# Performance work log

Measured on AMD Instinct MI355X. Metric: run time of the kernel, lower is better.

## Reference

```python
import jax, jax.numpy as jnp
import numpy as np

B, T, C = 128, 256, 256
K1, S1, T1 = 2, 2, 128   # conv scale 1: kernel, stride, output time steps
K2, S2, T2 = 4, 4, 64    # conv scale 2
TT = T + T1 + T2         # 448, concatenated time dim fed to TriU
EPS = 1e-5


def hardswish(x):
    return x * jnp.clip(x + 3.0, 0.0, 6.0) / 6.0


def setup_inputs() -> dict:
    key = jax.random.key(0)
    ks = jax.random.split(key, 9)
    return {
        "x": jax.random.normal(ks[0], (B, T, C), jnp.float32),
        "conv_w1": jax.random.normal(ks[1], (C, C, K1), jnp.float32) * 0.05,
        "conv_b1": jax.random.normal(ks[2], (C,), jnp.float32) * 0.05,
        "conv_w2": jax.random.normal(ks[3], (C, C, K2), jnp.float32) * 0.05,
        "conv_b2": jax.random.normal(ks[4], (C,), jnp.float32) * 0.05,
        "ln1_g": jnp.ones((T1, C), jnp.float32),
        "ln1_b": jnp.zeros((T1, C), jnp.float32),
        "ln2_g": jnp.ones((T2, C), jnp.float32),
        "ln2_b": jnp.zeros((T2, C), jnp.float32),
        "triu_w1": jax.random.normal(ks[5], (TT, TT), jnp.float32) * 0.05,
        "triu_b1": jax.random.normal(ks[6], (TT,), jnp.float32) * 0.05,
        "triu_w2": jax.random.normal(ks[7], (TT, TT), jnp.float32) * 0.05,
        "triu_b2": jax.random.normal(ks[8], (TT,), jnp.float32) * 0.05,
    }


def _layernorm2(x, g, b):
    # nn.LayerNorm([ts, C]): normalize jointly over last two dims of [B, ts, C]
    mu = jnp.mean(x, axis=(-2, -1), keepdims=True)
    var = jnp.var(x, axis=(-2, -1), keepdims=True)
    return (x - mu) * jax.lax.rsqrt(var + EPS) * g + b


def _conv1d(x_bct, w, b, stride):
    # x: [B, C, T], w: [Cout, Cin, K] -> [B, Cout, T_out], VALID padding
    y = jax.lax.conv_general_dilated(
        x_bct, w, window_strides=(stride,), padding='VALID',
        dimension_numbers=('NCH', 'OIH', 'NCH'))
    return y + b[None, :, None]


def reference(x, conv_w1, conv_b1, conv_w2, conv_b2,
              ln1_g, ln1_b, ln2_g, ln2_b,
              triu_w1, triu_b1, triu_w2, triu_b2):
    xc = jnp.transpose(x, (0, 2, 1))  # [B, C, T]
    f1 = _layernorm2(jnp.transpose(_conv1d(xc, conv_w1, conv_b1, S1), (0, 2, 1)), ln1_g, ln1_b)
    f2 = _layernorm2(jnp.transpose(_conv1d(xc, conv_w2, conv_b2, S2), (0, 2, 1)), ln2_g, ln2_b)
    cat = jnp.concatenate([x, f1, f2], axis=1)  # [B, TT, C]
    # TriU network on time axis: per-step Linear(i+1,1) == upper-triangular matmul
    z = jnp.transpose(cat, (0, 2, 1))  # [B, C, TT]
    mask = jnp.triu(jnp.ones((TT, TT), z.dtype))  # M[j,i]=w_i[j] for j<=i
    z = hardswish(z @ (triu_w1 * mask) + triu_b1)
    z = z @ (triu_w2 * mask) + triu_b2
    return jnp.transpose(z, (0, 2, 1))  # [B, TT, C]
```

## Files before the change

### kernel.cpp

```cpp
#include <hip/hip_runtime.h>
#include <hip/hip_bf16.h>

#define Bn   128
#define Tn   256
#define Cn   256
#define T1n  128
#define T2n  64
#define TTn  448
#define EPSf 1e-5f

typedef __attribute__((ext_vector_type(8))) short short8;
typedef __attribute__((ext_vector_type(4))) short short4v;
typedef __attribute__((ext_vector_type(4))) float f32x4;

__device__ __forceinline__ unsigned short f2b(float f) {
    union { __hip_bfloat16 h; unsigned short u; } cv;
    cv.h = __float2bfloat16(f);
    return cv.u;
}

__device__ __forceinline__ short8 cvt8(float4 a, float4 b) {
    short8 r;
    r[0] = (short)f2b(a.x); r[1] = (short)f2b(a.y); r[2] = (short)f2b(a.z); r[3] = (short)f2b(a.w);
    r[4] = (short)f2b(b.x); r[5] = (short)f2b(b.y); r[6] = (short)f2b(b.z); r[7] = (short)f2b(b.w);
    return r;
}

__global__ __launch_bounds__(256) void prep_all(
        const float* __restrict__ cw1, const float* __restrict__ cw2,
        const float* __restrict__ tw1, const float* __restrict__ tw2,
        const float* __restrict__ ln1g, const float* __restrict__ ln1b,
        const float* __restrict__ ln2g, const float* __restrict__ ln2b,
        unsigned short* __restrict__ w1rT, unsigned short* __restrict__ w2rT,
        unsigned short* __restrict__ wm1b, unsigned short* __restrict__ wm2b,
        float* __restrict__ gt1, float* __restrict__ bt1,
        float* __restrict__ gt2, float* __restrict__ bt2) {
    int idx = blockIdx.x * 256 + threadIdx.x;
    if (idx < 131072) {
        int co = idx >> 9, r = idx & 511, k = r >> 8, ci = r & 255;
        w1rT[idx] = f2b(cw1[(size_t)co * 512 + ci * 2 + k]);
    } else if ((idx -= 131072) < 262144) {
        int co = idx >> 10, r = idx & 1023, k = r >> 8, ci = r & 255;
        w2rT[idx] = f2b(cw2[(size_t)co * 1024 + ci * 4 + k]);
    } else if ((idx -= 262144) < 200704) {
        int i = idx / TTn, j = idx % TTn;
        wm1b[idx] = (j <= i) ? f2b(tw1[(size_t)j * TTn + i]) : (unsigned short)0;
    } else if ((idx -= 200704) < 200704) {
        int i = idx / TTn, j = idx % TTn;
        wm2b[idx] = (j <= i) ? f2b(tw2[(size_t)j * TTn + i]) : (unsigned short)0;
    } else if ((idx -= 200704) < 32768) {
        int c = idx >> 7, r = idx & 127;
        gt1[idx] = ln1g[(size_t)r * Cn + c];
    } else if ((idx -= 32768) < 32768) {
        int c = idx >> 7, r = idx & 127;
        bt1[idx] = ln1b[(size_t)r * Cn + c];
    } else if ((idx -= 32768) < 16384) {
        int c = idx >> 6, r = idx & 63;
        gt2[idx] = ln2g[(size_t)r * Cn + c];
    } else if ((idx -= 16384) < 16384) {
        int c = idx >> 6, r = idx & 63;
        bt2[idx] = ln2b[(size_t)r * Cn + c];
    }
}

__global__ __launch_bounds__(256) void xpose_kernel(const float* __restrict__ x,
                                                    unsigned short* __restrict__ catb) {
    __shared__ float tl[64][65];
    int b = blockIdx.z, t0 = blockIdx.y * 64, c0 = blockIdx.x * 64;
    const float* xp = x + (size_t)b * Tn * Cn;
    int lr = threadIdx.x >> 4;
    int lc = (threadIdx.x & 15) * 4;
#pragma unroll
    for (int rr = 0; rr < 4; ++rr) {
        int row = lr + rr * 16;
        float4 v = *(const float4*)(xp + (size_t)(t0 + row) * Cn + c0 + lc);
        tl[lc + 0][row] = v.x; tl[lc + 1][row] = v.y;
        tl[lc + 2][row] = v.z; tl[lc + 3][row] = v.w;
    }
    __syncthreads();
    int cr = threadIdx.x >> 2, tq = (threadIdx.x & 3) * 16;
    unsigned short* qp = catb + (size_t)b * (TTn * Cn) + (size_t)(c0 + cr) * TTn + t0 + tq;
    short8 o0, o1;
#pragma unroll
    for (int j = 0; j < 8; ++j) {
        o0[j] = (short)f2b(tl[cr][tq + j]);
        o1[j] = (short)f2b(tl[cr][tq + 8 + j]);
    }
    *(short8*)(qp) = o0;
    *(short8*)(qp + 8) = o1;
}

__global__ __launch_bounds__(256) void ln_apply_both(
        const float* __restrict__ c1t, const float* __restrict__ c2t,
        const float* __restrict__ gt1, const float* __restrict__ bt1,
        const float* __restrict__ gt2, const float* __restrict__ bt2,
        const float* __restrict__ ps1, const float* __restrict__ ps2,
        unsigned short* __restrict__ catb) {
    const int b = blockIdx.y, bx = blockIdx.x;
    const float *p, *g, *be;
    unsigned short* q;
    int LG, n, base;
    float S = 0.f, SS = 0.f;
    if (bx < 16) {
        n = Cn * T1n; LG = 7;
        p = c1t + (size_t)b * n; g = gt1; be = bt1;
        q = catb + (size_t)b * (TTn * Cn) + Tn;
#pragma unroll
        for (int s_ = 0; s_ < 4; ++s_) { S += ps1[b * 8 + s_ * 2]; SS += ps1[b * 8 + s_ * 2 + 1]; }
        base = bx * 2048;
    } else {
        n = Cn * T2n; LG = 6;
        p = c2t + (size_t)b * n; g = gt2; be = bt2;
        q = catb + (size_t)b * (TTn * Cn) + Tn + T1n;
#pragma unroll
        for (int s_ = 0; s_ < 2; ++s_) { S += ps2[b * 4 + s_ * 2]; SS += ps2[b * 4 + s_ * 2 + 1]; }
        base = (bx - 16) * 2048;
    }
    float mu = S / n;
    float rs = rsqrtf(SS / n - mu * mu + EPSf);

    int i = base + threadIdx.x * 8;
    int c = i >> LG, t = i & ((1 << LG) - 1);
    float4 v0 = *(const float4*)(p + i);
    float4 v1 = *(const float4*)(p + i + 4);
    float4 g0 = *(const float4*)(g + i);
    float4 g1 = *(const float4*)(g + i + 4);
    float4 b0 = *(const float4*)(be + i);
    float4 b1 = *(const float4*)(be + i + 4);
    float4 o0, o1;
    o0.x = fmaf((v0.x - mu) * rs, g0.x, b0.x);
    o0.y = fmaf((v0.y - mu) * rs, g0.y, b0.y);
    o0.z = fmaf((v0.z - mu) * rs, g0.z, b0.z);
    o0.w = fmaf((v0.w - mu) * rs, g0.w, b0.w);
    o1.x = fmaf((v1.x - mu) * rs, g1.x, b1.x);
    o1.y = fmaf((v1.y - mu) * rs, g1.y, b1.y);
    o1.z = fmaf((v1.z - mu) * rs, g1.z, b1.z);
    o1.w = fmaf((v1.w - mu) * rs, g1.w, b1.w);
    *(short8*)(q + (size_t)c * TTn + t) = cvt8(o0, o1);
}

template<bool AF32, int EPI>
__global__ __launch_bounds__(256)
void gemm_mfma(const void* __restrict__ Av, long astride, int lda,
               const unsigned short* __restrict__ Bsrc, long bstride, int ldb,
               const float* __restrict__ bias,
               void* __restrict__ Cv, long cstride, int ldc,
               int K, float* __restrict__ psout) {
    const int tid = threadIdx.x;
    const int lane = tid & 63;
    const int wid = tid >> 6;
    const int wr = wid >> 1, wc = wid & 1;
    const int bz = blockIdx.z;
    const int m0 = blockIdx.y * 64, n0 = blockIdx.x * 128;

    __shared__ unsigned short As[64 * 64];
    __shared__ unsigned short Bs[128 * 64];
    char* AsB = (char*)As;
    char* BsB = (char*)Bs;

    const int ar = tid >> 2, akq = tid & 3;
    const int bn_ = tid >> 1, bkh = (tid & 1) * 32;

    const float* Afp = (const float*)Av + (size_t)bz * astride + (size_t)(m0 + ar) * lda + akq * 16;
    const unsigned short* Ahp = (const unsigned short*)Av + (size_t)bz * astride + (size_t)(m0 + ar) * lda + akq * 16;
    const unsigned short* Bp = Bsrc + (size_t)bz * bstride + (size_t)(n0 + bn_) * ldb + bkh;

    const int awb = ar * 128 + akq * 32;
    const int aswz = (ar & 7) << 4;
    const int bwb = bn_ * 128 + bkh * 2;
    const int bswz = (bn_ & 7) << 4;

    short8 ra0, ra1, rb0, rb1, rb2, rb3;

    auto loadA = [&](int k0) {
        if constexpr (AF32) {
            const float* p = Afp + k0;
            float4 v0 = *(const float4*)(p);
            float4 v1 = *(const float4*)(p + 4);
            float4 v2 = *(const float4*)(p + 8);
            float4 v3 = *(const float4*)(p + 12);
            ra0 = cvt8(v0, v1);
            ra1 = cvt8(v2, v3);
        } else {
            ra0 = *(const short8*)(Ahp + k0);
            ra1 = *(const short8*)(Ahp + k0 + 8);
        }
    };
    auto loadB = [&](int k0) {
        rb0 = *(const short8*)(Bp + k0);
        rb1 = *(const short8*)(Bp + k0 + 8);
        rb2 = *(const short8*)(Bp + k0 + 16);
        rb3 = *(const short8*)(Bp + k0 + 24);
    };
    auto stage = [&]() {
        *(short8*)(AsB + ((awb) ^ aswz)) = ra0;
        *(short8*)(AsB + ((awb + 16) ^ aswz)) = ra1;
        *(short8*)(BsB + ((bwb) ^ bswz)) = rb0;
        *(short8*)(BsB + ((bwb + 16) ^ bswz)) = rb1;
        *(short8*)(BsB + ((bwb + 32) ^ bswz)) = rb2;
        *(short8*)(BsB + ((bwb + 48) ^ bswz)) = rb3;
    };

    const int fl = lane & 15;
    const int fkb = (lane >> 4) * 16;
    const int amb = (wr * 32 + fl) * 128;
    const int bnb = (wc * 64 + fl) * 128;
    const int fswz = (fl & 7) << 4;

    f32x4 acc[2][4];
#pragma unroll
    for (int i = 0; i < 2; ++i)
#pragma unroll
        for (int j = 0; j < 4; ++j) acc[i][j] = (f32x4){0.f, 0.f, 0.f, 0.f};

    const int nkt = (EPI == 0) ? (K >> 6) : ((m0 >> 6) + 1);

    loadA(0);
    loadB(0);
    for (int kt = 0; kt < nkt; ++kt) {
        __syncthreads();
        stage();
        __syncthreads();
        if (kt + 1 < nkt) { loadA((kt + 1) * 64); loadB((kt + 1) * 64); }
#pragma unroll
        for (int ks = 0; ks < 2; ++ks) {
            const int kb = ks * 64 + fkb;
            short8 af0 = *(const short8*)(AsB + ((amb + kb) ^ fswz));
            short8 af1 = *(const short8*)(AsB + ((amb + 2048 + kb) ^ fswz));
            short8 bf0 = *(const short8*)(BsB + ((bnb + kb) ^ fswz));
            short8 bf1 = *(const short8*)(BsB + ((bnb + 2048 + kb) ^ fswz));
            short8 bf2 = *(const short8*)(BsB + ((bnb + 4096 + kb) ^ fswz));
            short8 bf3 = *(const short8*)(BsB + ((bnb + 6144 + kb) ^ fswz));
            acc[0][0] = __builtin_amdgcn_mfma_f32_16x16x32_bf16(af0, bf0, acc[0][0], 0, 0, 0);
            acc[0][1] = __builtin_amdgcn_mfma_f32_16x16x32_bf16(af0, bf1, acc[0][1], 0, 0, 0);
            acc[0][2] = __builtin_amdgcn_mfma_f32_16x16x32_bf16(af0, bf2, acc[0][2], 0, 0, 0);
            acc[0][3] = __builtin_amdgcn_mfma_f32_16x16x32_bf16(af0, bf3, acc[0][3], 0, 0, 0);
            acc[1][0] = __builtin_amdgcn_mfma_f32_16x16x32_bf16(af1, bf0, acc[1][0], 0, 0, 0);
            acc[1][1] = __builtin_amdgcn_mfma_f32_16x16x32_bf16(af1, bf1, acc[1][1], 0, 0, 0);
            acc[1][2] = __builtin_amdgcn_mfma_f32_16x16x32_bf16(af1, bf2, acc[1][2], 0, 0, 0);
            acc[1][3] = __builtin_amdgcn_mfma_f32_16x16x32_bf16(af1, bf3, acc[1][3], 0, 0, 0);
        }
    }

    const int lrow = (lane >> 4) * 4;
    float s_ = 0.f, ss_ = 0.f;
#pragma unroll
    for (int mf = 0; mf < 2; ++mf) {
        const int trow = m0 + wr * 32 + mf * 16 + lrow;
#pragma unroll
        for (int nf = 0; nf < 4; ++nf) {
            const int col = n0 + wc * 64 + nf * 16 + fl;
            f32x4 v = acc[mf][nf];
            if (EPI == 0) {
                v += bias[col];
#pragma unroll
                for (int r = 0; r < 4; ++r) { s_ += v[r]; ss_ = fmaf(v[r], v[r], ss_); }
                float* Cb = (float*)Cv + (size_t)bz * cstride + (size_t)col * ldc + trow;
                *(f32x4*)Cb = v;
            } else if (EPI == 1) {
                f32x4 bv = *(const f32x4*)(bias + trow);
                v += bv;
                unsigned short* Cb = (unsigned short*)Cv + (size_t)bz * cstride + (size_t)col * ldc + trow;
                short4v pk;
#pragma unroll
                for (int r = 0; r < 4; ++r) {
                    float t = v[r];
                    float u = fminf(fmaxf(t + 3.f, 0.f), 6.f);
                    t = t * u * (1.f / 6.f);
                    pk[r] = (short)f2b(t);
                }
                *(short4v*)Cb = pk;
            } else {
                f32x4 bv = *(const f32x4*)(bias + trow);
                v += bv;
                float* Cb = (float*)Cv + (size_t)bz * cstride + (size_t)trow * ldc + col;
#pragma unroll
                for (int r = 0; r < 4; ++r) Cb[(size_t)r * ldc] = v[r];
            }
        }
    }

    if (EPI == 0) {
#pragma unroll
        for (int o = 32; o > 0; o >>= 1) { s_ += __shfl_down(s_, o); ss_ += __shfl_down(ss_, o); }
        __shared__ float rsm[8];
        if (lane == 0) { rsm[wid] = s_; rsm[wid + 4] = ss_; }
        __syncthreads();
        if (tid == 0) {
            float S = rsm[0] + rsm[1] + rsm[2] + rsm[3];
            float SS = rsm[4] + rsm[5] + rsm[6] + rsm[7];
            int nslots = gridDim.x * gridDim.y;
            int slot = blockIdx.y * gridDim.x + blockIdx.x;
            psout[((size_t)bz * nslots + slot) * 2 + 0] = S;
            psout[((size_t)bz * nslots + slot) * 2 + 1] = SS;
        }
    }
}

extern "C" void kernel_launch(void* const* d_in, const int* in_sizes, int n_in,
                              void* d_out, int out_size, void* d_ws, size_t ws_size,
                              hipStream_t stream) {
    const float* x    = (const float*)d_in[0];
    const float* cw1  = (const float*)d_in[1];
    const float* cb1  = (const float*)d_in[2];
    const float* cw2  = (const float*)d_in[3];
    const float* cb2  = (const float*)d_in[4];
    const float* ln1g = (const float*)d_in[5];
    const float* ln1b = (const float*)d_in[6];
    const float* ln2g = (const float*)d_in[7];
    const float* ln2b = (const float*)d_in[8];
    const float* tw1  = (const float*)d_in[9];
    const float* tb1  = (const float*)d_in[10];
    const float* tw2  = (const float*)d_in[11];
    const float* tb2  = (const float*)d_in[12];
    float* out = (float*)d_out;

    char* w = (char*)d_ws;
    unsigned short* catb = (unsigned short*)w;
    unsigned short* z1b  = (unsigned short*)(w + 29360128);
    float*          c1t  = (float*)(w + 58720256);
    float*          c2t  = (float*)(w + 75497472);
    unsigned short* w1rT = (unsigned short*)(w + 83886080);
    unsigned short* w2rT = (unsigned short*)(w + 84148224);
    unsigned short* wm1b = (unsigned short*)(w + 84672512);
    unsigned short* wm2b = (unsigned short*)(w + 85073920);
    float*          gt1  = (float*)(w + 85475328);
    float*          bt1  = (float*)(w + 85606400);
    float*          gt2  = (float*)(w + 85737472);
    float*          bt2  = (float*)(w + 85803008);
    float*          ps1  = (float*)(w + 85868544);
    float*          ps2  = (float*)(w + 85876736);

    prep_all<<<3488, 256, 0, stream>>>(cw1, cw2, tw1, tw2, ln1g, ln1b, ln2g, ln2b,
                                       w1rT, w2rT, wm1b, wm2b, gt1, bt1, gt2, bt2);

    xpose_kernel<<<dim3(4, 4, Bn), 256, 0, stream>>>(x, catb);

    gemm_mfma<true, 0><<<dim3(2, 2, Bn), 256, 0, stream>>>(
        x, 65536L, 512, w1rT, 0L, 512, cb1, c1t, (long)Cn * T1n, T1n, 512, ps1);
    gemm_mfma<true, 0><<<dim3(2, 1, Bn), 256, 0, stream>>>(
        x, 65536L, 1024, w2rT, 0L, 1024, cb2, c2t, (long)Cn * T2n, T2n, 1024, ps2);

    ln_apply_both<<<dim3(24, Bn), 256, 0, stream>>>(c1t, c2t, gt1, bt1, gt2, bt2, ps1, ps2, catb);

    gemm_mfma<false, 1><<<dim3(2, 7, Bn), 256, 0, stream>>>(
        wm1b, 0L, TTn, catb, (long)TTn * Cn, TTn, tb1, z1b, (long)TTn * Cn, TTn, TTn, nullptr);

    gemm_mfma<false, 2><<<dim3(2, 7, Bn), 256, 0, stream>>>(
        wm2b, 0L, TTn, z1b, (long)TTn * Cn, TTn, tb2, out, (long)TTn * Cn, Cn, TTn, nullptr);
}
```

Before: 113.6 us.

## Fuse transpose and conv GEMMs into one launch; use 128x128 tiles for TriU GEMMs

Merges the x transpose kernel and both strided-conv GEMMs into a single stage1 launch that dispatches on blockIdx.y, which removes two kernel launches and lets the three pieces of work run concurrently. The TriU GEMMs move from 64x128 to 128x128 tiles with a 4x4 MFMA fragment per wave, raising data reuse per block. To support this, the masked weight matrices are padded to 512 rows with zeros and the workspace offsets are shifted. The larger tile uses more registers and LDS and skips less of the triangular work, since it works at 128-row granularity.

New measurement: 141.6 us. 24.7% more time.

```diff
diff --git a/kernel.cpp b/kernel.cpp
--- a/kernel.cpp
+++ b/kernel.cpp
@@ -42,13 +42,13 @@
     } else if ((idx -= 131072) < 262144) {
         int co = idx >> 10, r = idx & 1023, k = r >> 8, ci = r & 255;
         w2rT[idx] = f2b(cw2[(size_t)co * 1024 + ci * 4 + k]);
-    } else if ((idx -= 262144) < 200704) {
+    } else if ((idx -= 262144) < 229376) {
         int i = idx / TTn, j = idx % TTn;
-        wm1b[idx] = (j <= i) ? f2b(tw1[(size_t)j * TTn + i]) : (unsigned short)0;
-    } else if ((idx -= 200704) < 200704) {
+        wm1b[idx] = (i < TTn && j <= i) ? f2b(tw1[(size_t)j * TTn + i]) : (unsigned short)0;
+    } else if ((idx -= 229376) < 229376) {
         int i = idx / TTn, j = idx % TTn;
-        wm2b[idx] = (j <= i) ? f2b(tw2[(size_t)j * TTn + i]) : (unsigned short)0;
-    } else if ((idx -= 200704) < 32768) {
+        wm2b[idx] = (i < TTn && j <= i) ? f2b(tw2[(size_t)j * TTn + i]) : (unsigned short)0;
+    } else if ((idx -= 229376) < 32768) {
         int c = idx >> 7, r = idx & 127;
         gt1[idx] = ln1g[(size_t)r * Cn + c];
     } else if ((idx -= 32768) < 32768) {
@@ -63,10 +63,11 @@
     }
 }
 
-__global__ __launch_bounds__(256) void xpose_kernel(const float* __restrict__ x,
-                                                    unsigned short* __restrict__ catb) {
-    __shared__ float tl[64][65];
-    int b = blockIdx.z, t0 = blockIdx.y * 64, c0 = blockIdx.x * 64;
+
+__device__ __forceinline__ void xpose_body(char* smem, const float* __restrict__ x,
+                                           unsigned short* __restrict__ catb,
+                                           int b, int t0, int c0) {
+    float (*tl)[65] = (float(*)[65])smem;
     const float* xp = x + (size_t)b * Tn * Cn;
     int lr = threadIdx.x >> 4;
     int lc = (threadIdx.x & 15) * 4;
@@ -88,6 +89,145 @@
     }
     *(short8*)(qp) = o0;
     *(short8*)(qp + 8) = o1;
+}
+
+__device__ __forceinline__ void conv_body(char* smem,
+        const float* __restrict__ x, int lda,
+        const unsigned short* __restrict__ Bw,
+        const float* __restrict__ bias,
+        float* __restrict__ Cout, long cstride, int ldc, int K,
+        float* __restrict__ psout, int slot, int nslots,
+        int m0, int n0, int bz) {
+    char* AsB = smem;
+    char* BsB = smem + 8192;
+    const int tid = threadIdx.x;
+    const int lane = tid & 63;
+    const int wid = tid >> 6;
+    const int wr = wid >> 1, wc = wid & 1;
+
+    const int ar = tid >> 2, akq = tid & 3;
+    const int bn_ = tid >> 1, bkh = (tid & 1) * 32;
+
+    const float* Afp = x + (size_t)bz * (Tn * Cn) + (size_t)(m0 + ar) * lda + akq * 16;
+    const unsigned short* Bp = Bw + (size_t)(n0 + bn_) * K + bkh;
+
+    const int awb = ar * 128 + akq * 32;
+    const int aswz = (ar & 7) << 4;
+    const int bwb = bn_ * 128 + bkh * 2;
+    const int bswz = (bn_ & 7) << 4;
+
+    short8 ra0, ra1, rb0, rb1, rb2, rb3;
+    auto loadA = [&](int k0) {
+        const float* p = Afp + k0;
+        float4 v0 = *(const float4*)(p);
+        float4 v1 = *(const float4*)(p + 4);
+        float4 v2 = *(const float4*)(p + 8);
+        float4 v3 = *(const float4*)(p + 12);
+        ra0 = cvt8(v0, v1);
+        ra1 = cvt8(v2, v3);
+    };
+    auto loadB = [&](int k0) {
+        rb0 = *(const short8*)(Bp + k0);
+        rb1 = *(const short8*)(Bp + k0 + 8);
+        rb2 = *(const short8*)(Bp + k0 + 16);
+        rb3 = *(const short8*)(Bp + k0 + 24);
+    };
+
+    const int fl = lane & 15;
+    const int fkb = (lane >> 4) * 16;
+    const int amb = (wr * 32 + fl) * 128;
+    const int bnb = (wc * 64 + fl) * 128;
+    const int fswz = (fl & 7) << 4;
+
+    f32x4 acc[2][4];
+#pragma unroll
+    for (int i = 0; i < 2; ++i)
+#pragma unroll
+        for (int j = 0; j < 4; ++j) acc[i][j] = (f32x4){0.f, 0.f, 0.f, 0.f};
+
+    const int nkt = K >> 6;
+    loadA(0); loadB(0);
+    for (int kt = 0; kt < nkt; ++kt) {
+        __syncthreads();
+        *(short8*)(AsB + ((awb) ^ aswz)) = ra0;
+        *(short8*)(AsB + ((awb + 16) ^ aswz)) = ra1;
+        *(short8*)(BsB + ((bwb) ^ bswz)) = rb0;
+        *(short8*)(BsB + ((bwb + 16) ^ bswz)) = rb1;
+        *(short8*)(BsB + ((bwb + 32) ^ bswz)) = rb2;
+        *(short8*)(BsB + ((bwb + 48) ^ bswz)) = rb3;
+        __syncthreads();
+        if (kt + 1 < nkt) { loadA((kt + 1) * 64); loadB((kt + 1) * 64); }
+#pragma unroll
+        for (int ks = 0; ks < 2; ++ks) {
+            const int kb = ks * 64 + fkb;
+            short8 af0 = *(const short8*)(AsB + ((amb + kb) ^ fswz));
+            short8 af1 = *(const short8*)(AsB + ((amb + 2048 + kb) ^ fswz));
+            short8 bf0 = *(const short8*)(BsB + ((bnb + kb) ^ fswz));
+            short8 bf1 = *(const short8*)(BsB + ((bnb + 2048 + kb) ^ fswz));
+            short8 bf2 = *(const short8*)(BsB + ((bnb + 4096 + kb) ^ fswz));
+            short8 bf3 = *(const short8*)(BsB + ((bnb + 6144 + kb) ^ fswz));
+            acc[0][0] = __builtin_amdgcn_mfma_f32_16x16x32_bf16(af0, bf0, acc[0][0], 0, 0, 0);
+            acc[0][1] = __builtin_amdgcn_mfma_f32_16x16x32_bf16(af0, bf1, acc[0][1], 0, 0, 0);
+            acc[0][2] = __builtin_amdgcn_mfma_f32_16x16x32_bf16(af0, bf2, acc[0][2], 0, 0, 0);
+            acc[0][3] = __builtin_amdgcn_mfma_f32_16x16x32_bf16(af0, bf3, acc[0][3], 0, 0, 0);
+            acc[1][0] = __builtin_amdgcn_mfma_f32_16x16x32_bf16(af1, bf0, acc[1][0], 0, 0, 0);
+            acc[1][1] = __builtin_amdgcn_mfma_f32_16x16x32_bf16(af1, bf1, acc[1][1], 0, 0, 0);
+            acc[1][2] = __builtin_amdgcn_mfma_f32_16x16x32_bf16(af1, bf2, acc[1][2], 0, 0, 0);
+            acc[1][3] = __builtin_amdgcn_mfma_f32_16x16x32_bf16(af1, bf3, acc[1][3], 0, 0, 0);
+        }
+    }
+
+    const int lrow = (lane >> 4) * 4;
+    float s_ = 0.f, ss_ = 0.f;
+#pragma unroll
+    for (int mf = 0; mf < 2; ++mf) {
+        const int trow = m0 + wr * 32 + mf * 16 + lrow;
+#pragma unroll
+        for (int nf = 0; nf < 4; ++nf) {
+            const int col = n0 + wc * 64 + nf * 16 + fl;
+            f32x4 v = acc[mf][nf];
+            v += bias[col];
+#pragma unroll
+            for (int r = 0; r < 4; ++r) { s_ += v[r]; ss_ = fmaf(v[r], v[r], ss_); }
+            float* Cb = Cout + (size_t)bz * cstride + (size_t)col * ldc + trow;
+            *(f32x4*)Cb = v;
+        }
+    }
+
+#pragma unroll
+    for (int o = 32; o > 0; o >>= 1) { s_ += __shfl_down(s_, o); ss_ += __shfl_down(ss_, o); }
+    __syncthreads();
+    float* rsm = (float*)smem;
+    if (lane == 0) { rsm[wid] = s_; rsm[wid + 4] = ss_; }
+    __syncthreads();
+    if (tid == 0) {
+        float S = rsm[0] + rsm[1] + rsm[2] + rsm[3];
+        float SS = rsm[4] + rsm[5] + rsm[6] + rsm[7];
+        psout[((size_t)bz * nslots + slot) * 2 + 0] = S;
+        psout[((size_t)bz * nslots + slot) * 2 + 1] = SS;
+    }
+}
+
+__global__ __launch_bounds__(256) void stage1(
+        const float* __restrict__ x,
+        const unsigned short* __restrict__ w1rT, const unsigned short* __restrict__ w2rT,
+        const float* __restrict__ cb1, const float* __restrict__ cb2,
+        float* __restrict__ c1t, float* __restrict__ c2t,
+        unsigned short* __restrict__ catb,
+        float* __restrict__ ps1, float* __restrict__ ps2) {
+    __shared__ alignas(16) char smem[25600];
+    const int y = blockIdx.y, xb = blockIdx.x, bz = blockIdx.z;
+    if (y >= 3) {
+        xpose_body(smem, x, catb, bz, (y - 3) * 64, xb * 64);
+    } else if (y < 2) {
+        if (xb < 2)
+            conv_body(smem, x, 512, w1rT, cb1, c1t, (long)Cn * T1n, T1n, 512,
+                      ps1, y * 2 + xb, 4, y * 64, xb * 128, bz);
+    } else {
+        if (xb < 2)
+            conv_body(smem, x, 1024, w2rT, cb2, c2t, (long)Cn * T2n, T2n, 1024,
+                      ps2, xb, 2, 0, xb * 128, bz);
+    }
 }
 
 __global__ __launch_bounds__(256) void ln_apply_both(
@@ -139,128 +279,91 @@
     *(short8*)(q + (size_t)c * TTn + t) = cvt8(o0, o1);
 }
 
-template<bool AF32, int EPI>
+template<int EPI>
 __global__ __launch_bounds__(256)
-void gemm_mfma(const void* __restrict__ Av, long astride, int lda,
-               const unsigned short* __restrict__ Bsrc, long bstride, int ldb,
-               const float* __restrict__ bias,
-               void* __restrict__ Cv, long cstride, int ldc,
-               int K, float* __restrict__ psout) {
+void gemm128(const unsigned short* __restrict__ Asrc,
+             const unsigned short* __restrict__ Bsrc, long bstride,
+             const float* __restrict__ bias,
+             void* __restrict__ Cv, long cstride) {
     const int tid = threadIdx.x;
     const int lane = tid & 63;
     const int wid = tid >> 6;
     const int wr = wid >> 1, wc = wid & 1;
     const int bz = blockIdx.z;
-    const int m0 = blockIdx.y * 64, n0 = blockIdx.x * 128;
-
-    __shared__ unsigned short As[64 * 64];
+    const int m0 = blockIdx.y * 128, n0 = blockIdx.x * 128;
+
+    __shared__ unsigned short As[128 * 64];
     __shared__ unsigned short Bs[128 * 64];
     char* AsB = (char*)As;
     char* BsB = (char*)Bs;
 
-    const int ar = tid >> 2, akq = tid & 3;
-    const int bn_ = tid >> 1, bkh = (tid & 1) * 32;
-
-    const float* Afp = (const float*)Av + (size_t)bz * astride + (size_t)(m0 + ar) * lda + akq * 16;
-    const unsigned short* Ahp = (const unsigned short*)Av + (size_t)bz * astride + (size_t)(m0 + ar) * lda + akq * 16;
-    const unsigned short* Bp = Bsrc + (size_t)bz * bstride + (size_t)(n0 + bn_) * ldb + bkh;
-
-    const int awb = ar * 128 + akq * 32;
-    const int aswz = (ar & 7) << 4;
-    const int bwb = bn_ * 128 + bkh * 2;
-    const int bswz = (bn_ & 7) << 4;
-
-    short8 ra0, ra1, rb0, rb1, rb2, rb3;
-
-    auto loadA = [&](int k0) {
-        if constexpr (AF32) {
-            const float* p = Afp + k0;
-            float4 v0 = *(const float4*)(p);
-            float4 v1 = *(const float4*)(p + 4);
-            float4 v2 = *(const float4*)(p + 8);
-            float4 v3 = *(const float4*)(p + 12);
-            ra0 = cvt8(v0, v1);
-            ra1 = cvt8(v2, v3);
-        } else {
-            ra0 = *(const short8*)(Ahp + k0);
-            ra1 = *(const short8*)(Ahp + k0 + 8);
-        }
-    };
-    auto loadB = [&](int k0) {
-        rb0 = *(const short8*)(Bp + k0);
-        rb1 = *(const short8*)(Bp + k0 + 8);
-        rb2 = *(const short8*)(Bp + k0 + 16);
-        rb3 = *(const short8*)(Bp + k0 + 24);
-    };
-    auto stage = [&]() {
-        *(short8*)(AsB + ((awb) ^ aswz)) = ra0;
-        *(short8*)(AsB + ((awb + 16) ^ aswz)) = ra1;
-        *(short8*)(BsB + ((bwb) ^ bswz)) = rb0;
-        *(short8*)(BsB + ((bwb + 16) ^ bswz)) = rb1;
-        *(short8*)(BsB + ((bwb + 32) ^ bswz)) = rb2;
-        *(short8*)(BsB + ((bwb + 48) ^ bswz)) = rb3;
+    const int srow = tid >> 1, skh = (tid & 1) * 32;
+    const unsigned short* Ap = Asrc + (size_t)(m0 + srow) * TTn + skh;
+    const unsigned short* Bp = Bsrc + (size_t)bz * bstride + (size_t)(n0 + srow) * TTn + skh;
+    const int swb = srow * 128 + skh * 2;
+    const int sswz = (srow & 7) << 4;
+
+    short8 ra[4], rb[4];
+    auto loadAB = [&](int k0) {
+#pragma unroll
+        for (int j = 0; j < 4; ++j) {
+            ra[j] = *(const short8*)(Ap + k0 + j * 8);
+            rb[j] = *(const short8*)(Bp + k0 + j * 8);
+        }
     };
 
     const int fl = lane & 15;
     const int fkb = (lane >> 4) * 16;
-    const int amb = (wr * 32 + fl) * 128;
-    const int bnb = (wc * 64 + fl) * 128;
     const int fswz = (fl & 7) << 4;
 
-    f32x4 acc[2][4];
-#pragma unroll
-    for (int i = 0; i < 2; ++i)
+    f32x4 acc[4][4];
+#pragma unroll
+    for (int i = 0; i < 4; ++i)
 #pragma unroll
         for (int j = 0; j < 4; ++j) acc[i][j] = (f32x4){0.f, 0.f, 0.f, 0.f};
 
-    const int nkt = (EPI == 0) ? (K >> 6) : ((m0 >> 6) + 1);
-
-    loadA(0);
-    loadB(0);
+    const int nkt = min(7, (m0 >> 6) + 2);
+
+    loadAB(0);
     for (int kt = 0; kt < nkt; ++kt) {
         __syncthreads();
-        stage();
+#pragma unroll
+        for (int j = 0; j < 4; ++j) {
+            *(short8*)(AsB + ((swb + j * 16) ^ sswz)) = ra[j];
+            *(short8*)(BsB + ((swb + j * 16) ^ sswz)) = rb[j];
+        }
         __syncthreads();
-        if (kt + 1 < nkt) { loadA((kt + 1) * 64); loadB((kt + 1) * 64); }
+        if (kt + 1 < nkt) loadAB((kt + 1) * 64);
 #pragma unroll
         for (int ks = 0; ks < 2; ++ks) {
             const int kb = ks * 64 + fkb;
-            short8 af0 = *(const short8*)(AsB + ((amb + kb) ^ fswz));
-            short8 af1 = *(const short8*)(AsB + ((amb + 2048 + kb) ^ fswz));
-            short8 bf0 = *(const short8*)(BsB + ((bnb + kb) ^ fswz));
-            short8 bf1 = *(const short8*)(BsB + ((bnb + 2048 + kb) ^ fswz));
-            short8 bf2 = *(const short8*)(BsB + ((bnb + 4096 + kb) ^ fswz));
-            short8 bf3 = *(const short8*)(BsB + ((bnb + 6144 + kb) ^ fswz));
-            acc[0][0] = __builtin_amdgcn_mfma_f32_16x16x32_bf16(af0, bf0, acc[0][0], 0, 0, 0);
-            acc[0][1] = __builtin_amdgcn_mfma_f32_16x16x32_bf16(af0, bf1, acc[0][1], 0, 0, 0);
-            acc[0][2] = __builtin_amdgcn_mfma_f32_16x16x32_bf16(af0, bf2, acc[0][2], 0, 0, 0);
-            acc[0][3] = __builtin_amdgcn_mfma_f32_16x16x32_bf16(af0, bf3, acc[0][3], 0, 0, 0);
-            acc[1][0] = __builtin_amdgcn_mfma_f32_16x16x32_bf16(af1, bf0, acc[1][0], 0, 0, 0);
-            acc[1][1] = __builtin_amdgcn_mfma_f32_16x16x32_bf16(af1, bf1, acc[1][1], 0, 0, 0);
-            acc[1][2] = __builtin_amdgcn_mfma_f32_16x16x32_bf16(af1, bf2, acc[1][2], 0, 0, 0);
-            acc[1][3] = __builtin_amdgcn_mfma_f32_16x16x32_bf16(af1, bf3, acc[1][3], 0, 0, 0);
+            short8 af[4], bf[4];
+#pragma unroll
+            for (int mf = 0; mf < 4; ++mf)
+                af[mf] = *(const short8*)(AsB + (((wr * 64 + mf * 16 + fl) * 128 + kb) ^ fswz));
+#pragma unroll
+            for (int nf = 0; nf < 4; ++nf)
+                bf[nf] = *(const short8*)(BsB + (((wc * 64 + nf * 16 + fl) * 128 + kb) ^ fswz));
+#pragma unroll
+            for (int mf = 0; mf < 4; ++mf)
+#pragma unroll
+                for (int nf = 0; nf < 4; ++nf)
+                    acc[mf][nf] = __builtin_amdgcn_mfma_f32_16x16x32_bf16(af[mf], bf[nf], acc[mf][nf], 0, 0, 0);
         }
     }
 
     const int lrow = (lane >> 4) * 4;
-    float s_ = 0.f, ss_ = 0.f;
-#pragma unroll
-    for (int mf = 0; mf < 2; ++mf) {
-        const int trow = m0 + wr * 32 + mf * 16 + lrow;
+#pragma unroll
+    for (int mf = 0; mf < 4; ++mf) {
+        const int trow = m0 + wr * 64 + mf * 16 + lrow;
+        if (trow >= TTn) continue;
+        f32x4 bv = *(const f32x4*)(bias + trow);
 #pragma unroll
         for (int nf = 0; nf < 4; ++nf) {
             const int col = n0 + wc * 64 + nf * 16 + fl;
-            f32x4 v = acc[mf][nf];
-            if (EPI == 0) {
-                v += bias[col];
-#pragma unroll
-                for (int r = 0; r < 4; ++r) { s_ += v[r]; ss_ = fmaf(v[r], v[r], ss_); }
-                float* Cb = (float*)Cv + (size_t)bz * cstride + (size_t)col * ldc + trow;
-                *(f32x4*)Cb = v;
-            } else if (EPI == 1) {
-                f32x4 bv = *(const f32x4*)(bias + trow);
-                v += bv;
-                unsigned short* Cb = (unsigned short*)Cv + (size_t)bz * cstride + (size_t)col * ldc + trow;
+            f32x4 v = acc[mf][nf] + bv;
+            if (EPI == 1) {
+                unsigned short* Cb = (unsigned short*)Cv + (size_t)bz * cstride + (size_t)col * TTn + trow;
                 short4v pk;
 #pragma unroll
                 for (int r = 0; r < 4; ++r) {
@@ -271,28 +374,10 @@
                 }
                 *(short4v*)Cb = pk;
             } else {
-                f32x4 bv = *(const f32x4*)(bias + trow);
-                v += bv;
-                float* Cb = (float*)Cv + (size_t)bz * cstride + (size_t)trow * ldc + col;
-#pragma unroll
-                for (int r = 0; r < 4; ++r) Cb[(size_t)r * ldc] = v[r];
+                float* Cb = (float*)Cv + (size_t)bz * cstride + (size_t)trow * Cn + col;
+#pragma unroll
+                for (int r = 0; r < 4; ++r) Cb[(size_t)r * Cn] = v[r];
             }
-        }
-    }
-
-    if (EPI == 0) {
-#pragma unroll
-        for (int o = 32; o > 0; o >>= 1) { s_ += __shfl_down(s_, o); ss_ += __shfl_down(ss_, o); }
-        __shared__ float rsm[8];
-        if (lane == 0) { rsm[wid] = s_; rsm[wid + 4] = ss_; }
-        __syncthreads();
-        if (tid == 0) {
-            float S = rsm[0] + rsm[1] + rsm[2] + rsm[3];
-            float SS = rsm[4] + rsm[5] + rsm[6] + rsm[7];
-            int nslots = gridDim.x * gridDim.y;
-            int slot = blockIdx.y * gridDim.x + blockIdx.x;
-            psout[((size_t)bz * nslots + slot) * 2 + 0] = S;
-            psout[((size_t)bz * nslots + slot) * 2 + 1] = SS;
         }
     }
 }
@@ -323,29 +408,24 @@
     unsigned short* w1rT = (unsigned short*)(w + 83886080);
     unsigned short* w2rT = (unsigned short*)(w + 84148224);
     unsigned short* wm1b = (unsigned short*)(w + 84672512);
-    unsigned short* wm2b = (unsigned short*)(w + 85073920);
-    float*          gt1  = (float*)(w + 85475328);
-    float*          bt1  = (float*)(w + 85606400);
-    float*          gt2  = (float*)(w + 85737472);
-    float*          bt2  = (float*)(w + 85803008);
-    float*          ps1  = (float*)(w + 85868544);
-    float*          ps2  = (float*)(w + 85876736);
-
-    prep_all<<<3488, 256, 0, stream>>>(cw1, cw2, tw1, tw2, ln1g, ln1b, ln2g, ln2b,
+    unsigned short* wm2b = (unsigned short*)(w + 85131264);
+    float*          gt1  = (float*)(w + 85590016);
+    float*          bt1  = (float*)(w + 85721088);
+    float*          gt2  = (float*)(w + 85852160);
+    float*          bt2  = (float*)(w + 85917696);
+    float*          ps1  = (float*)(w + 85983232);
+    float*          ps2  = (float*)(w + 85987328);
+
+    prep_all<<<3713, 256, 0, stream>>>(cw1, cw2, tw1, tw2, ln1g, ln1b, ln2g, ln2b,
                                        w1rT, w2rT, wm1b, wm2b, gt1, bt1, gt2, bt2);
 
-    xpose_kernel<<<dim3(4, 4, Bn), 256, 0, stream>>>(x, catb);
-
-    gemm_mfma<true, 0><<<dim3(2, 2, Bn), 256, 0, stream>>>(
-        x, 65536L, 512, w1rT, 0L, 512, cb1, c1t, (long)Cn * T1n, T1n, 512, ps1);
-    gemm_mfma<true, 0><<<dim3(2, 1, Bn), 256, 0, stream>>>(
-        x, 65536L, 1024, w2rT, 0L, 1024, cb2, c2t, (long)Cn * T2n, T2n, 1024, ps2);
+    stage1<<<dim3(4, 7, Bn), 256, 0, stream>>>(x, w1rT, w2rT, cb1, cb2, c1t, c2t, catb, ps1, ps2);
 
     ln_apply_both<<<dim3(24, Bn), 256, 0, stream>>>(c1t, c2t, gt1, bt1, gt2, bt2, ps1, ps2, catb);
 
-    gemm_mfma<false, 1><<<dim3(2, 7, Bn), 256, 0, stream>>>(
-        wm1b, 0L, TTn, catb, (long)TTn * Cn, TTn, tb1, z1b, (long)TTn * Cn, TTn, TTn, nullptr);
-
-    gemm_mfma<false, 2><<<dim3(2, 7, Bn), 256, 0, stream>>>(
-        wm2b, 0L, TTn, z1b, (long)TTn * Cn, TTn, tb2, out, (long)TTn * Cn, Cn, TTn, nullptr);
-}
+    gemm128<1><<<dim3(2, 4, Bn), 256, 0, stream>>>(
+        wm1b, catb, (long)TTn * Cn, tb1, z1b, (long)TTn * Cn);
+
+    gemm128<2><<<dim3(2, 4, Bn), 256, 0, stream>>>(
+        wm2b, z1b, (long)TTn * Cn, tb2, out, (long)TTn * Cn);
+}
```
